# Performance work log

Hardware: AMD Instinct MI355X
Metric: run time of the kernel (lower is better)

Reference implementation:

```python
import jax, jax.numpy as jnp
import numpy as np

NUM_HEADS = 16
D_MODEL = 1024
HEAD_DIM = D_MODEL // NUM_HEADS
NEG_BIG = 1e10


def setup_inputs() -> dict:
    key = jax.random.key(0)
    k1, k2, k3 = jax.random.split(key, 3)
    B, T = 2, 2048
    from_tensor = jax.random.normal(k1, (B, T, D_MODEL), dtype=jnp.float32)
    init = 0.02
    Wqkv = jax.random.normal(k2, (D_MODEL, 3 * D_MODEL), dtype=jnp.float32) * init
    bqkv = jnp.zeros((3 * D_MODEL,), dtype=jnp.float32)
    Wproj = jax.random.normal(k3, (D_MODEL, D_MODEL), dtype=jnp.float32) * init
    bproj = jnp.zeros((D_MODEL,), dtype=jnp.float32)
    return {"from_tensor": from_tensor, "Wqkv": Wqkv, "bqkv": bqkv,
            "Wproj": Wproj, "bproj": bproj}


def reference(from_tensor, Wqkv, bqkv, Wproj, bproj):
    B, T, D = from_tensor.shape
    H, hd = NUM_HEADS, D // NUM_HEADS
    qkv = from_tensor @ Wqkv + bqkv                      # [B,T,3D]
    q, k, v = jnp.split(qkv, 3, axis=-1)
    def heads(x):  # [B,T,D] -> [B,H,T,hd]
        return x.reshape(B, T, H, hd).transpose(0, 2, 1, 3)
    q, k, v = heads(q), heads(k), heads(v)
    present = jnp.stack([k, v], axis=1)                  # [B,2,H,T,hd]
    scores = jnp.einsum('bhqd,bhkd->bhqk', q, k)         # [B,H,T,T]
    scores = scores * jax.lax.rsqrt(jnp.float32(hd))
    # faithful mask: m = i > j - ns + nd (strict; diagonal masked)
    nd = ns = T
    i = jnp.arange(nd)[:, None]
    j = jnp.arange(ns)
    m = (i > j - ns + nd).astype(scores.dtype)           # [T,T]
    scores = scores * m - NEG_BIG * (1.0 - m)
    probs = jax.nn.softmax(scores, axis=-1)
    ctx = jnp.einsum('bhqk,bhkd->bhqd', probs, v)        # [B,H,T,hd]
    ctx = ctx.transpose(0, 2, 1, 3).reshape(B, T, D)
    out = ctx @ Wproj + bproj                            # [B,T,D]
    return out, present
```

## Files before the change

kernel.cpp:

```cpp
#include <hip/hip_runtime.h>
#include <hip/hip_bf16.h>
#include <cstdint>

typedef __bf16 bf16_t;
typedef __bf16 bf16x4 __attribute__((ext_vector_type(4)));
typedef __bf16 bf16x8 __attribute__((ext_vector_type(8)));
typedef float  f32x4  __attribute__((ext_vector_type(4)));

#define MFMA16(a,b,c) __builtin_amdgcn_mfma_f32_16x16x32_bf16(a,b,c,0,0,0)

#if __has_builtin(__builtin_amdgcn_exp2f)
#define EXP2(x) __builtin_amdgcn_exp2f(x)
#else
#define EXP2(x) exp2f(x)
#endif

__device__ __forceinline__ void gl_lds16(const void* g, void* l){
    __builtin_amdgcn_global_load_lds(
        (const __attribute__((address_space(1))) void*)g,
        (__attribute__((address_space(3))) void*)l, 16, 0, 0);
}

__global__ void k_cvt(const float* __restrict__ src, bf16_t* __restrict__ dst, int n4){
    int stride = gridDim.x * blockDim.x;
    for (int i = blockIdx.x * blockDim.x + threadIdx.x; i < n4; i += stride){
        float4 v = ((const float4*)src)[i];
        bf16x4 o = { (bf16_t)v.x, (bf16_t)v.y, (bf16_t)v.z, (bf16_t)v.w };
        ((bf16x4*)dst)[i] = o;
    }
}

__global__ void k_transpose_cvt(const float* __restrict__ src, bf16_t* __restrict__ dst,
                                int R, int C){
    __shared__ bf16_t tile[32][33];
    int c0 = blockIdx.x * 32, r0 = blockIdx.y * 32;
    int tx = threadIdx.x & 31, g = threadIdx.x >> 5;
#pragma unroll
    for (int p = 0; p < 4; ++p){
        int r = g + p * 8;
        tile[r][tx] = (bf16_t)src[(size_t)(r0 + r) * C + c0 + tx];
    }
    __syncthreads();
#pragma unroll
    for (int p = 0; p < 4; ++p){
        int rr = g + p * 8;
        dst[(size_t)(c0 + rr) * R + r0 + tx] = tile[tx][rr];
    }
}

template<int MODE>
__global__ void k_gemm(const bf16_t* __restrict__ A, const bf16_t* __restrict__ Bt,
                       const float* __restrict__ bias,
                       float* __restrict__ Cout,
                       bf16_t* __restrict__ qws, bf16_t* __restrict__ kws,
                       bf16_t* __restrict__ vws,
                       int M, int N, int K){
    __shared__ bf16_t sA[128 * 64];
    __shared__ bf16_t sB[128 * 64];
    int m0 = blockIdx.x * 128, n0 = blockIdx.y * 128;
    int tid = threadIdx.x, lane = tid & 63, w = tid >> 6;
    int lr = lane & 15, lg = lane >> 4;
    int wm = (w >> 1) * 64, wn = (w & 1) * 64;
    f32x4 acc[4][4] = {};

    int srow = lane >> 3;
    int scol = ((lane & 7) ^ srow) * 8;

    for (int k0 = 0; k0 < K; k0 += 64){
#pragma unroll
        for (int p = 0; p < 4; ++p){
            int c = w + p * 4;
            gl_lds16(A  + (size_t)(m0 + c * 8 + srow) * K + k0 + scol, &sA[c * 512]);
            gl_lds16(Bt + (size_t)(n0 + c * 8 + srow) * K + k0 + scol, &sB[c * 512]);
        }
        __syncthreads();
#pragma unroll
        for (int ks = 0; ks < 2; ++ks){
            bf16x8 af[4], bfm[4];
            int ca = ((ks * 4 + lg) ^ (lr & 7)) * 8;
#pragma unroll
            for (int i = 0; i < 4; ++i){
                af[i]  = *(const bf16x8*)(sA + (wm + i * 16 + lr) * 64 + ca);
                bfm[i] = *(const bf16x8*)(sB + (wn + i * 16 + lr) * 64 + ca);
            }
#pragma unroll
            for (int i = 0; i < 4; ++i)
#pragma unroll
                for (int j = 0; j < 4; ++j)
                    acc[i][j] = MFMA16(af[i], bfm[j], acc[i][j]);
        }
        __syncthreads();
    }

#pragma unroll
    for (int j = 0; j < 4; ++j){
        int n = n0 + wn + j * 16 + lr;
        float bv = bias[n];
#pragma unroll
        for (int i = 0; i < 4; ++i){
            int mbase = m0 + wm + i * 16 + lg * 4;
#pragma unroll
            for (int r = 0; r < 4; ++r){
                float cv = acc[i][j][r] + bv;
                int m = mbase + r;
                if (MODE == 1){
                    Cout[(size_t)m * N + n] = cv;
                } else {
                    int b = m >> 11, t = m & 2047;
                    int sec = n >> 10, rem = n & 1023;
                    int h = rem >> 6, d = rem & 63;
                    size_t hbase = (((size_t)b * 16 + h) * 2048 + t) * 64;
                    if (sec == 0){
                        qws[hbase + d] = (bf16_t)cv;
                    } else if (sec == 1){
                        kws[hbase + (d ^ ((t & 7) << 3))] = (bf16_t)cv;
                        Cout[((((size_t)b * 2 + 0) * 16 + h) * 2048 + t) * 64 + d] = cv;
                    } else {
                        int tl = t & 63;
                        int sp = (tl & 0x23) | ((tl & 0x0C) << 1) | ((tl & 0x10) >> 2);
                        vws[(((size_t)b * 16 + h) * 64 + d) * 2048 + (t & ~63)
                            + (sp ^ ((d & 7) << 3))] = (bf16_t)cv;
                        Cout[((((size_t)b * 2 + 1) * 16 + h) * 2048 + t) * 64 + d] = cv;
                    }
                }
            }
        }
    }
}

__device__ __forceinline__ void stage_kv8(const bf16_t* khead, const bf16_t* vhead,
                                          bf16_t* sKb, bf16_t* sVb,
                                          int kv0, int w, int lane){
    gl_lds16(khead + (size_t)(kv0 + w * 8 + (lane >> 3)) * 64 + (lane & 7) * 8,
             sKb + w * 512);
    gl_lds16(vhead + (size_t)(w * 8 + (lane >> 3)) * 2048 + kv0 + (lane & 7) * 8,
             sVb + w * 512);
}

__global__ __launch_bounds__(512, 4) void k_flash(const bf16_t* __restrict__ qb,
                        const bf16_t* __restrict__ kb, const bf16_t* __restrict__ vt,
                        bf16_t* __restrict__ ctx){
    __shared__ bf16_t sK[3][4096];
    __shared__ bf16_t sV[3][4096];
    int bid = blockIdx.x;
    int x = bid & 7, p = bid >> 3;
    int c = p & 31, pass = p >> 5;
    int bh = x * 4 + pass * 2 + (c >> 4);
    int qt = pass ? 15 - (c & 15) : (c & 15);
    int b = bh >> 4, h = bh & 15;
    int tid = threadIdx.x, lane = tid & 63, w = tid >> 6;
    int lr = lane & 15, lg = lane >> 4;
    int q0 = qt * 128;
    int nkt = 2 * qt + 2;
    const bf16_t* qhead = qb + (size_t)bh * 131072;
    const bf16_t* khead = kb + (size_t)bh * 131072;
    const bf16_t* vhead = vt + (size_t)bh * 131072;
    const float SC = 0.18033688f;

    bf16x8 aq0, aq1;
    {
        const bf16_t* p2 = qhead + (size_t)(q0 + w * 16 + lr) * 64 + lg * 8;
        bf16x8 r0 = *(const bf16x8*)p2, r1 = *(const bf16x8*)(p2 + 32);
#pragma unroll
        for (int j = 0; j < 8; ++j){
            aq0[j] = (bf16_t)((float)r0[j] * SC);
            aq1[j] = (bf16_t)((float)r1[j] * SC);
        }
    }
    float lsum = 0.f;
    f32x4 oacc[4] = {};

    bf16_t *cK = sK[0], *cV = sV[0];
    bf16_t *nK = sK[1], *nV = sV[1];
    bf16_t *xK = sK[2], *xV = sV[2];
    stage_kv8(khead, vhead, cK, cV, 0, w, lane);
    stage_kv8(khead, vhead, nK, nV, 64, w, lane);

    for (int kt = 0; kt < nkt; ++kt){
        asm volatile("s_waitcnt vmcnt(2)" ::: "memory");
        __builtin_amdgcn_s_barrier();
        {
            int nt = kt + 2; if (nt > nkt - 1) nt = nkt - 1;
            stage_kv8(khead, vhead, xK, xV, nt * 64, w, lane);
        }

        bf16x8 kf[8], vf[8];
#pragma unroll
        for (int cf = 0; cf < 4; ++cf){
            kf[cf * 2]     = *(const bf16x8*)(&cK[(cf * 16 + lr) * 64 + ((lg * 8) ^ ((lr & 7) << 3))]);
            kf[cf * 2 + 1] = *(const bf16x8*)(&cK[(cf * 16 + lr) * 64 + ((32 + lg * 8) ^ ((lr & 7) << 3))]);
        }
#pragma unroll
        for (int ks = 0; ks < 2; ++ks)
#pragma unroll
            for (int df = 0; df < 4; ++df)
                vf[ks * 4 + df] = *(const bf16x8*)(&cV[(df * 16 + lr) * 64 + ((ks * 32 + lg * 8) ^ ((lr & 7) << 3))]);

        f32x4 s[4];
        __builtin_amdgcn_s_setprio(1);
#pragma unroll
        for (int cf = 0; cf < 4; ++cf){
            f32x4 a = {};
            a = MFMA16(kf[cf * 2],     aq0, a);
            a = MFMA16(kf[cf * 2 + 1], aq1, a);
            s[cf] = a;
        }
        __builtin_amdgcn_s_setprio(0);
        if (kt >= 2 * qt){
            int qi = q0 + w * 16 + lr;
            int kvg = kt * 64;
#pragma unroll
            for (int cf = 0; cf < 4; ++cf){
                int kvb = kvg + cf * 16 + lg * 4;
#pragma unroll
                for (int r = 0; r < 4; ++r)
                    if (qi <= kvb + r) s[cf][r] = -1e10f;
            }
        }
        __builtin_amdgcn_sched_barrier(0);
        float rsum = 0.f;
        bf16x8 ap0, ap1;
#pragma unroll
        for (int cf = 0; cf < 4; ++cf)
#pragma unroll
            for (int r = 0; r < 4; ++r){
                float pv = EXP2(s[cf][r]);
                rsum += pv;
                if (cf < 2) ap0[(cf & 1) * 4 + r] = (bf16_t)pv;
                else        ap1[(cf & 1) * 4 + r] = (bf16_t)pv;
            }
        lsum += rsum;
        __builtin_amdgcn_s_setprio(1);
#pragma unroll
        for (int ks = 0; ks < 2; ++ks){
            bf16x8 ap = ks ? ap1 : ap0;
#pragma unroll
            for (int df = 0; df < 4; ++df)
                oacc[df] = MFMA16(ap, vf[ks * 4 + df], oacc[df]);
        }
        __builtin_amdgcn_s_setprio(0);
        bf16_t* tK = cK; bf16_t* tV = cV;
        cK = nK; cV = nV; nK = xK; nV = xV; xK = tK; xV = tV;
    }
    asm volatile("s_waitcnt vmcnt(0)" ::: "memory");

    float lt = lsum;
    lt += __shfl_xor(lt, 16);
    lt += __shfl_xor(lt, 32);
    float ls0 = __shfl(lt, lg * 4 + 0);
    float ls1 = __shfl(lt, lg * 4 + 1);
    float ls2 = __shfl(lt, lg * 4 + 2);
    float ls3 = __shfl(lt, lg * 4 + 3);
#pragma unroll
    for (int df = 0; df < 4; ++df){
        int d = df * 16 + lr;
        int tb = q0 + w * 16 + lg * 4;
        size_t base = ((size_t)b * 2048 + tb) * 1024 + h * 64 + d;
        ctx[base]        = (bf16_t)(oacc[df][0] / ls0);
        ctx[base + 1024] = (bf16_t)(oacc[df][1] / ls1);
        ctx[base + 2048] = (bf16_t)(oacc[df][2] / ls2);
        ctx[base + 3072] = (bf16_t)(oacc[df][3] / ls3);
    }
}

__global__ void k_row0fix(const bf16_t* __restrict__ vt, bf16_t* __restrict__ ctx){
    int bh = blockIdx.y;
    int b = bh >> 4, h = bh & 15;
    int lane = threadIdx.x & 63, w = threadIdx.x >> 6;
    int d = blockIdx.x * 4 + w;
    const bf16_t* row = vt + ((size_t)bh * 64 + d) * 2048;
    float s = 0.f;
#pragma unroll
    for (int k = 0; k < 4; ++k){
        bf16x8 v = *(const bf16x8*)(row + (lane + k * 64) * 8);
#pragma unroll
        for (int j = 0; j < 8; ++j) s += (float)v[j];
    }
#pragma unroll
    for (int off = 1; off < 64; off <<= 1) s += __shfl_xor(s, off);
    if (lane == 0)
        ctx[(size_t)b * 2048 * 1024 + h * 64 + d] = (bf16_t)(s * (1.f / 2048.f));
}

extern "C" void kernel_launch(void* const* d_in, const int* in_sizes, int n_in,
                              void* d_out, int out_size, void* d_ws, size_t ws_size,
                              hipStream_t stream){
    const float* X     = (const float*)d_in[0];
    const float* Wqkv  = (const float*)d_in[1];
    const float* bqkv  = (const float*)d_in[2];
    const float* Wproj = (const float*)d_in[3];
    const float* bproj = (const float*)d_in[4];
    float* out = (float*)d_out;
    float* present = out + 4194304;

    char* ws = (char*)d_ws;
    bf16_t* Xb     = (bf16_t*)(ws);
    bf16_t* WqkvT  = (bf16_t*)(ws + 8388608);
    bf16_t* WprojT = (bf16_t*)(ws + 14680064);
    bf16_t* Qb     = (bf16_t*)(ws + 16777216);
    bf16_t* Kb     = (bf16_t*)(ws + 25165824);
    bf16_t* Vt     = (bf16_t*)(ws + 33554432);
    bf16_t* CTXb   = (bf16_t*)(ws + 41943040);

    k_cvt<<<2048, 256, 0, stream>>>(X, Xb, 4194304 / 4);
    k_transpose_cvt<<<dim3(3072 / 32, 1024 / 32), 256, 0, stream>>>(Wqkv, WqkvT, 1024, 3072);
    k_transpose_cvt<<<dim3(1024 / 32, 1024 / 32), 256, 0, stream>>>(Wproj, WprojT, 1024, 1024);
    k_gemm<0><<<dim3(32, 24), 256, 0, stream>>>(Xb, WqkvT, bqkv, present, Qb, Kb, Vt, 4096, 3072, 1024);
    k_flash<<<512, 512, 0, stream>>>(Qb, Kb, Vt, CTXb);
    k_row0fix<<<dim3(16, 32), 256, 0, stream>>>(Vt, CTXb);
    k_gemm<1><<<dim3(32, 8), 256, 0, stream>>>(CTXb, WprojT, bproj, out, nullptr, nullptr, nullptr, 4096, 1024, 1024);
}
```

Baseline: 101.1 us.

## Double-buffer GEMM shared-memory tiles with async prefetch two stages ahead

The QKV and output-projection GEMM now keeps two LDS buffers for A and B tiles and issues global-to-LDS loads for the next stages while MFMAs run on the current one, replacing a load/sync/compute/sync loop. It uses explicit vmcnt waits and raw barriers, plus s_setprio around the MFMA block and launch bounds of 256 threads with 2 blocks. The goal is to hide global memory latency in the GEMMs. Costs are doubled LDS per block (64KB), which may limit occupancy, and redundant tail loads that clamp to the last tile.

```diff
diff --git a/kernel.cpp b/kernel.cpp
--- a/kernel.cpp
+++ b/kernel.cpp
@@ -49,14 +49,15 @@
 }
 
 template<int MODE>
-__global__ void k_gemm(const bf16_t* __restrict__ A, const bf16_t* __restrict__ Bt,
+__global__ __launch_bounds__(256, 2) void k_gemm(
+                       const bf16_t* __restrict__ A, const bf16_t* __restrict__ Bt,
                        const float* __restrict__ bias,
                        float* __restrict__ Cout,
                        bf16_t* __restrict__ qws, bf16_t* __restrict__ kws,
                        bf16_t* __restrict__ vws,
                        int M, int N, int K){
-    __shared__ bf16_t sA[128 * 64];
-    __shared__ bf16_t sB[128 * 64];
+    __shared__ bf16_t sA[2][128 * 64];
+    __shared__ bf16_t sB[2][128 * 64];
     int m0 = blockIdx.x * 128, n0 = blockIdx.y * 128;
     int tid = threadIdx.x, lane = tid & 63, w = tid >> 6;
     int lr = lane & 15, lg = lane >> 4;
@@ -66,30 +67,44 @@
     int srow = lane >> 3;
     int scol = ((lane & 7) ^ srow) * 8;
 
-    for (int k0 = 0; k0 < K; k0 += 64){
+    auto stage = [&](int bu, int k0){
 #pragma unroll
         for (int p = 0; p < 4; ++p){
             int c = w + p * 4;
-            gl_lds16(A  + (size_t)(m0 + c * 8 + srow) * K + k0 + scol, &sA[c * 512]);
-            gl_lds16(Bt + (size_t)(n0 + c * 8 + srow) * K + k0 + scol, &sB[c * 512]);
-        }
-        __syncthreads();
+            gl_lds16(A  + (size_t)(m0 + c * 8 + srow) * K + k0 + scol, &sA[bu][c * 512]);
+            gl_lds16(Bt + (size_t)(n0 + c * 8 + srow) * K + k0 + scol, &sB[bu][c * 512]);
+        }
+    };
+
+    int niter = K >> 6;
+    stage(0, 0);
+    stage(1, 64);
+
+    for (int kt = 0; kt < niter; ++kt){
+        asm volatile("s_waitcnt vmcnt(8)" ::: "memory");
+        __builtin_amdgcn_s_barrier();
+        const bf16_t* cA = sA[kt & 1];
+        const bf16_t* cB = sB[kt & 1];
 #pragma unroll
         for (int ks = 0; ks < 2; ++ks){
             bf16x8 af[4], bfm[4];
             int ca = ((ks * 4 + lg) ^ (lr & 7)) * 8;
 #pragma unroll
             for (int i = 0; i < 4; ++i){
-                af[i]  = *(const bf16x8*)(sA + (wm + i * 16 + lr) * 64 + ca);
-                bfm[i] = *(const bf16x8*)(sB + (wn + i * 16 + lr) * 64 + ca);
+                af[i]  = *(const bf16x8*)(cA + (wm + i * 16 + lr) * 64 + ca);
+                bfm[i] = *(const bf16x8*)(cB + (wn + i * 16 + lr) * 64 + ca);
             }
+            __builtin_amdgcn_s_setprio(1);
 #pragma unroll
             for (int i = 0; i < 4; ++i)
 #pragma unroll
                 for (int j = 0; j < 4; ++j)
                     acc[i][j] = MFMA16(af[i], bfm[j], acc[i][j]);
-        }
-        __syncthreads();
+            __builtin_amdgcn_s_setprio(0);
+        }
+        __builtin_amdgcn_s_barrier();
+        int nk = kt + 2; if (nk > niter - 1) nk = niter - 1;
+        stage(kt & 1, nk * 64);
     }
 
 #pragma unroll
@@ -126,6 +141,7 @@
             }
         }
     }
+    asm volatile("s_waitcnt vmcnt(0)" ::: "memory");
 }
 
 __device__ __forceinline__ void stage_kv8(const bf16_t* khead, const bf16_t* vhead,
```

Result: slower. 110.8 us (+9.6%).
